# Optimization experiments

Hardware: AMD Instinct MI355X
Metric: run time of the kernel (lower is better)

## Reference

```python
import jax, jax.numpy as jnp
import numpy as np

N_NODES = 100000
N_ANGLES = 1000000
SCALAR_DIM = 128
ANGLE_ATTR_DIM = 2
HIDDEN = 64


def setup_inputs() -> dict:
    key = jax.random.key(0)
    ks = jax.random.split(key, 10)
    x = jax.random.normal(ks[0], (N_NODES, SCALAR_DIM), dtype=jnp.float32)
    triple_index = jax.random.randint(ks[1], (3, N_ANGLES), 0, N_NODES, dtype=jnp.int64)
    triple_attr = jax.random.normal(ks[2], (N_ANGLES, ANGLE_ATTR_DIM), dtype=jnp.float32)
    d_in = SCALAR_DIM * 2 + ANGLE_ATTR_DIM  # 258
    W1 = jax.random.normal(ks[3], (d_in, HIDDEN), dtype=jnp.float32) / np.sqrt(d_in)
    b1 = jnp.zeros((HIDDEN,), dtype=jnp.float32)
    W2 = jax.random.normal(ks[4], (HIDDEN, HIDDEN), dtype=jnp.float32) / np.sqrt(HIDDEN)
    b2 = jnp.zeros((HIDDEN,), dtype=jnp.float32)
    W3 = jax.random.normal(ks[5], (HIDDEN, SCALAR_DIM), dtype=jnp.float32) / np.sqrt(HIDDEN)
    b3 = jnp.zeros((SCALAR_DIM,), dtype=jnp.float32)
    # o3.Linear 128x0e -> 128x0e: bias-free dense linear with 1/sqrt(fan_in) norm
    Wout = jax.random.normal(ks[6], (SCALAR_DIM, SCALAR_DIM), dtype=jnp.float32) / np.sqrt(SCALAR_DIM)
    return {"x": x, "triple_index": triple_index, "triple_attr": triple_attr,
            "W1": W1, "b1": b1, "W2": W2, "b2": b2, "W3": W3, "b3": b3, "Wout": Wout}


def reference(x, triple_index, triple_attr, W1, b1, W2, b2, W3, b3, Wout):
    num_nodes = x.shape[0]
    x_scalar = x[:, :SCALAR_DIM]
    i, j, k = triple_index[0], triple_index[1], triple_index[2]
    # gather endpoints, concat with angle attrs: [E, 2*scalar_dim + 2]
    angle_input = jnp.concatenate([x_scalar[i], x_scalar[k], triple_attr], axis=-1)
    h = jax.nn.silu(angle_input @ W1 + b1)
    h = jax.nn.silu(h @ W2 + b2)
    msgs = h @ W3 + b3  # [E, scalar_dim]
    # scatter-mean by j
    sums = jax.ops.segment_sum(msgs, j, num_segments=num_nodes)
    cnts = jax.ops.segment_sum(jnp.ones((msgs.shape[0],), msgs.dtype), j, num_segments=num_nodes)
    aggr = sums / jnp.maximum(cnts, 1.0)[:, None]
    return aggr @ Wout
```

## Files before the change

### kernel.cpp

```cpp
#include <hip/hip_runtime.h>

#define NN 100000
#define NE 1000000
#define NBLK_SCAN 391

typedef float f4 __attribute__((ext_vector_type(4)));
typedef float f2 __attribute__((ext_vector_type(2)));
typedef _Float16 h8 __attribute__((ext_vector_type(8)));

__device__ __forceinline__ float silu(float v) {
    return v / (1.0f + __expf(-v));
}

#define O_SUMS   0
#define O_CNT    6400000
#define O_OFF    6500000
#define O_BSUM   6600000
#define O_BPRE   6600512
#define O_PERM   6601024
#define O_XA     7601024
#define O_XB     10801024
#define O_W3W    14001024
#define O_W2T    14009344

#define NODEPRE_B 3125
#define HIST_B    3907
#define W3W_B     33
#define PREP_B    (NODEPRE_B + HIST_B + W3W_B + 1)

__global__ __launch_bounds__(256) void k_prep(
    const float* __restrict__ x, const int* __restrict__ tj,
    const float* __restrict__ W1, const float* __restrict__ W2,
    const float* __restrict__ W3, const float* __restrict__ b3,
    const float* __restrict__ Wout,
    _Float16* __restrict__ XA, _Float16* __restrict__ XB,
    int* __restrict__ C, float* __restrict__ W3W, _Float16* __restrict__ W2t) {
    __shared__ float X[32][128];
    const int b = blockIdx.x;
    const int t = threadIdx.x;
    if (b < NODEPRE_B) {
        const int n0 = b * 32;
        const f4* xs = (const f4*)(x + (size_t)n0 * 128);
        f4* Xs = (f4*)&X[0][0];
#pragma unroll
        for (int q = 0; q < 4; ++q) Xs[t + 256 * q] = xs[t + 256 * q];
        __syncthreads();
        const int w = t >> 6, lane = t & 63;
        float aA[8], aB[8];
#pragma unroll
        for (int m = 0; m < 8; ++m) { aA[m] = 0.f; aB[m] = 0.f; }
        for (int d = 0; d < 128; ++d) {
            float wA = W1[d * 64 + lane];
            float wB = W1[(128 + d) * 64 + lane];
#pragma unroll
            for (int m = 0; m < 8; ++m) {
                float xv = X[w * 8 + m][d];
                aA[m] += xv * wA;
                aB[m] += xv * wB;
            }
        }
#pragma unroll
        for (int m = 0; m < 8; ++m) {
            XA[(size_t)(n0 + w * 8 + m) * 64 + lane] = (_Float16)aA[m];
            XB[(size_t)(n0 + w * 8 + m) * 64 + lane] = (_Float16)aB[m];
        }
    } else if (b < NODEPRE_B + HIST_B) {
        int e = (b - NODEPRE_B) * 256 + t;
        if (e < NE) atomicAdd(&C[tj[e]], 1);
    } else if (b < NODEPRE_B + HIST_B + W3W_B) {
        const int row = (b - NODEPRE_B - HIST_B) * 2 + (t >> 7);
        const int c = t & 127;
        if (row < 65) {
            const float* arow = (row < 64) ? (W3 + row * 128) : b3;
            float acc = 0.f;
            for (int d = 0; d < 128; ++d) acc += arow[d] * Wout[d * 128 + c];
            W3W[row * 128 + c] = acc;
        }
    } else {
#pragma unroll
        for (int u = 0; u < 16; ++u) {
            const int idx = t * 16 + u;
            const int n = idx >> 6, k = idx & 63;
            W2t[idx] = (_Float16)W2[k * 64 + n];
        }
    }
}

__global__ __launch_bounds__(256) void k_scan_local(const int* __restrict__ C,
                                                    int* __restrict__ offv,
                                                    int* __restrict__ Bsum) {
    __shared__ int s[256];
    const int t = threadIdx.x;
    const int gid = blockIdx.x * 256 + t;
    const int v = (gid < NN) ? C[gid] : 0;
    s[t] = v;
    __syncthreads();
    for (int off = 1; off < 256; off <<= 1) {
        int add = (t >= off) ? s[t - off] : 0;
        __syncthreads();
        s[t] += add;
        __syncthreads();
    }
    if (gid < NN) offv[gid] = s[t] - v;
    if (t == 255) Bsum[blockIdx.x] = s[255];
}

__global__ __launch_bounds__(512) void k_scan_block(const int* __restrict__ Bsum,
                                                    int* __restrict__ Bpre) {
    __shared__ int s[512];
    const int t = threadIdx.x;
    const int v = (t < NBLK_SCAN) ? Bsum[t] : 0;
    s[t] = v;
    __syncthreads();
    for (int off = 1; off < 512; off <<= 1) {
        int add = (t >= off) ? s[t - off] : 0;
        __syncthreads();
        s[t] += add;
        __syncthreads();
    }
    if (t < NBLK_SCAN) Bpre[t] = s[t] - v;
}

__global__ __launch_bounds__(256) void k_scatter(const int* __restrict__ tj,
                                                 const int* __restrict__ Bpre,
                                                 int* __restrict__ offv,
                                                 int* __restrict__ perm) {
    int e = blockIdx.x * 256 + threadIdx.x;
    if (e < NE) {
        int j = tj[e];
        int p = Bpre[j >> 8] + atomicAdd(&offv[j], 1);
        perm[p] = e;
    }
}

__global__ __launch_bounds__(256, 8) void k_edge(
    const int* __restrict__ ti, const int* __restrict__ tj, const int* __restrict__ tk,
    const int* __restrict__ perm, const float* __restrict__ attr,
    const _Float16* __restrict__ XA, const _Float16* __restrict__ XB,
    const float* __restrict__ W1, const float* __restrict__ b1,
    const _Float16* __restrict__ W2t, const float* __restrict__ b2,
    float* __restrict__ sums) {
    __shared__ __align__(16) char SBraw[64 * 68 * 4];
    __shared__ int JL[64];
    __shared__ int RS[66];
    __shared__ int nruns_s;

    _Float16* H1h = (_Float16*)SBraw;
    float* M = (float*)SBraw;

    const int t = threadIdx.x;
    const int w = t >> 6;
    const int lane = t & 63;
    const int EB = blockIdx.x * 64;

    {
        const int el = t >> 2;
        const int q = t & 3;
        const int e = perm[EB + el];
        const int i = ti[e];
        const int k = tk[e];
        if (q == 0) JL[el] = tj[e];
        f2 at = ((const f2*)attr)[e];
        const _Float16* xa = XA + (size_t)i * 64 + q * 16;
        const _Float16* xb = XB + (size_t)k * 64 + q * 16;
        h8 va0 = ((const h8*)xa)[0], va1 = ((const h8*)xa)[1];
        h8 vb0 = ((const h8*)xb)[0], vb1 = ((const h8*)xb)[1];
        float fa[16], fb[16];
#pragma unroll
        for (int n = 0; n < 8; ++n) {
            fa[n] = (float)va0[n]; fa[8 + n] = (float)va1[n];
            fb[n] = (float)vb0[n]; fb[8 + n] = (float)vb1[n];
        }
        const float* c0 = W1 + 256 * 64 + q * 16;
        const float* c1 = W1 + 257 * 64 + q * 16;
        const float* bq = b1 + q * 16;
        _Float16 hrow[16];
#pragma unroll
        for (int m4 = 0; m4 < 4; ++m4) {
            f4 vc0 = ((const f4*)c0)[m4];
            f4 vc1 = ((const f4*)c1)[m4];
            f4 vbq = ((const f4*)bq)[m4];
#pragma unroll
            for (int n = 0; n < 4; ++n) {
                const int idx = m4 * 4 + n;
                float pre = fa[idx] + fb[idx] + at[0] * vc0[n] + at[1] * vc1[n] + vbq[n];
                hrow[idx] = (_Float16)silu(pre);
            }
        }
        h8 s0, s1;
#pragma unroll
        for (int n = 0; n < 8; ++n) { s0[n] = hrow[n]; s1[n] = hrow[8 + n]; }
        _Float16* row = H1h + el * 72 + q * 16;
        ((h8*)row)[0] = s0;
        ((h8*)row)[1] = s1;
    }
    __syncthreads();

    const int r15 = lane & 15;
    const int blk = lane >> 4;
    float h2v[16];
    {
        const _Float16* H1w = H1h + (w * 16) * 72;
        h8 a0 = *(const h8*)(H1w + r15 * 72 + blk * 8);
        h8 a1 = *(const h8*)(H1w + r15 * 72 + 32 + blk * 8);
#pragma unroll
        for (int ncol = 0; ncol < 4; ++ncol) {
            const _Float16* Wn = W2t + (ncol * 16 + r15) * 64 + blk * 8;
            h8 b0 = *(const h8*)(Wn);
            h8 b1v = *(const h8*)(Wn + 32);
            const float bc = b2[ncol * 16 + r15];
            f4 acc = {bc, bc, bc, bc};
            acc = __builtin_amdgcn_mfma_f32_16x16x32_f16(a0, b0, acc, 0, 0, 0);
            acc = __builtin_amdgcn_mfma_f32_16x16x32_f16(a1, b1v, acc, 0, 0, 0);
#pragma unroll
            for (int reg = 0; reg < 4; ++reg) h2v[ncol * 4 + reg] = silu(acc[reg]);
        }
    }
    __syncthreads();

#pragma unroll
    for (int ncol = 0; ncol < 4; ++ncol)
#pragma unroll
        for (int reg = 0; reg < 4; ++reg)
            M[(w * 16 + blk * 4 + reg) * 68 + ncol * 16 + r15] = h2v[ncol * 4 + reg];
    if (t < 64) {
        bool head = (t == 0) || (JL[t] != JL[t - 1]);
        unsigned long long mask = __ballot(head);
        if (head) {
            int rank = __popcll(mask & ((1ull << t) - 1ull));
            RS[rank] = t;
        }
        if (t == 0) {
            int nr = __popcll(mask);
            nruns_s = nr;
            RS[nr] = 64;
        }
    }
    __syncthreads();

    {
        const int col = t & 63;
        const int q4 = t >> 6;
        const int nr = nruns_s;
        for (int rid = q4; rid < nr; rid += 4) {
            const int s0 = RS[rid];
            const int s1 = RS[rid + 1];
            float a = 0.f;
            for (int rr = s0; rr < s1; ++rr) a += M[rr * 68 + col];
            atomicAdd(&sums[(size_t)JL[s0] * 64 + col], a);
        }
    }
}

__global__ __launch_bounds__(256) void k_out(const float* __restrict__ sums,
                                             const int* __restrict__ C,
                                             const float* __restrict__ W3W,
                                             float* __restrict__ out) {
    __shared__ float S[32][64];
    __shared__ float bs[32];
    const int t = threadIdx.x;
    const int n0 = blockIdx.x * 32;
    const f4* ss = (const f4*)(sums + (size_t)n0 * 64);
    f4* Ss = (f4*)&S[0][0];
#pragma unroll
    for (int q = 0; q < 2; ++q) {
        const int fidx = t + 256 * q;
        const int row = fidx >> 4;
        const int cn = C[n0 + row];
        const float sc = (cn > 0) ? 1.0f / (float)cn : 0.0f;
        f4 v = ss[fidx];
#pragma unroll
        for (int n = 0; n < 4; ++n) v[n] *= sc;
        Ss[fidx] = v;
    }
    if (t < 32) bs[t] = (C[n0 + t] > 0) ? 1.0f : 0.0f;
    __syncthreads();
    const int w = t >> 6, lane = t & 63;
    const float* bout = W3W + 64 * 128;
    float a0[8], a1[8];
#pragma unroll
    for (int m = 0; m < 8; ++m) { a0[m] = 0.f; a1[m] = 0.f; }
    for (int d = 0; d < 64; ++d) {
        float w0 = W3W[d * 128 + lane];
        float w1 = W3W[d * 128 + 64 + lane];
#pragma unroll
        for (int m = 0; m < 8; ++m) {
            float sv = S[w * 8 + m][d];
            a0[m] += sv * w0;
            a1[m] += sv * w1;
        }
    }
    const float bo0 = bout[lane], bo1 = bout[64 + lane];
#pragma unroll
    for (int m = 0; m < 8; ++m) {
        const int node = n0 + w * 8 + m;
        const float b = bs[w * 8 + m];
        out[(size_t)node * 128 + lane] = a0[m] + b * bo0;
        out[(size_t)node * 128 + 64 + lane] = a1[m] + b * bo1;
    }
}

extern "C" void kernel_launch(void* const* d_in, const int* in_sizes, int n_in,
                              void* d_out, int out_size, void* d_ws, size_t ws_size,
                              hipStream_t stream) {
    const float* x    = (const float*)d_in[0];
    const int*   idx  = (const int*)d_in[1];
    const float* attr = (const float*)d_in[2];
    const float* W1   = (const float*)d_in[3];
    const float* b1   = (const float*)d_in[4];
    const float* W2   = (const float*)d_in[5];
    const float* b2   = (const float*)d_in[6];
    const float* W3   = (const float*)d_in[7];
    const float* b3   = (const float*)d_in[8];
    const float* Wout = (const float*)d_in[9];
    float* out = (float*)d_out;

    const int* ti = idx;
    const int* tj = idx + NE;
    const int* tk = idx + 2 * NE;

    float* ws   = (float*)d_ws;
    float* sums = ws + O_SUMS;
    int*   C    = (int*)(ws + O_CNT);
    int*   offv = (int*)(ws + O_OFF);
    int*   Bsum = (int*)(ws + O_BSUM);
    int*   Bpre = (int*)(ws + O_BPRE);
    int*   perm = (int*)(ws + O_PERM);
    _Float16* XA  = (_Float16*)(ws + O_XA);
    _Float16* XB  = (_Float16*)(ws + O_XB);
    float* W3W  = ws + O_W3W;
    _Float16* W2t = (_Float16*)(ws + O_W2T);

    hipMemsetAsync(sums, 0, (size_t)(6400000 + 100000) * sizeof(float), stream);

    hipLaunchKernelGGL(k_prep,       dim3(PREP_B), dim3(256), 0, stream,
                       x, tj, W1, W2, W3, b3, Wout, XA, XB, C, W3W, W2t);
    hipLaunchKernelGGL(k_scan_local, dim3(NBLK_SCAN), dim3(256), 0, stream, C, offv, Bsum);
    hipLaunchKernelGGL(k_scan_block, dim3(1), dim3(512), 0, stream, Bsum, Bpre);
    hipLaunchKernelGGL(k_scatter,    dim3(3907), dim3(256), 0, stream, tj, Bpre, offv, perm);
    hipLaunchKernelGGL(k_edge,       dim3(15625), dim3(256), 0, stream,
                       ti, tj, tk, perm, attr, XA, XB, W1, b1, W2t, b2, sums);
    hipLaunchKernelGGL(k_out,        dim3(3125), dim3(256), 0, stream, sums, C, W3W, out);
}
```

Before: 440.6 us.

## Use split-fp16 MFMA for node projection and fuse prep, scan and zeroing stages

Replaces the scalar FP32 node pre-projection (x @ W1 halves) with MFMA 16x16x32 fp16 instructions, using a hi/lo split of both x and W1 to keep near-fp32 accuracy. The histogram and weight prep stay in a first kernel. A new mid kernel merges the node projection with the local scan and with zeroing of the sums buffer, so the large memset is gone. The block-level scan is folded into k_scatter as a per-block wavefront scan, and nontemporal loads are added for the edge index streams. Together these cut launch count and FP32 ALU work, at the cost of three MFMAs per tile and some redundant scan work in every scatter block.

```diff
diff --git a/kernel.cpp b/kernel.cpp
--- a/kernel.cpp
+++ b/kernel.cpp
@@ -16,59 +16,34 @@
 #define O_CNT    6400000
 #define O_OFF    6500000
 #define O_BSUM   6600000
-#define O_BPRE   6600512
-#define O_PERM   6601024
-#define O_XA     7601024
-#define O_XB     10801024
-#define O_W3W    14001024
-#define O_W2T    14009344
-
-#define NODEPRE_B 3125
-#define HIST_B    3907
-#define W3W_B     33
-#define PREP_B    (NODEPRE_B + HIST_B + W3W_B + 1)
-
-__global__ __launch_bounds__(256) void k_prep(
-    const float* __restrict__ x, const int* __restrict__ tj,
+#define O_PERM   6600512
+#define O_XA     7600512
+#define O_XB     10800512
+#define O_W3W    14000512
+#define O_W2T    14008832
+#define O_W1TH   14010880
+#define O_W1TR   14019072
+
+#define HIST_B  3907
+#define W3W_B   33
+#define PREP0_B (HIST_B + W3W_B + 1 + 8)
+#define NPRE_B  1563
+#define MID_B   (NPRE_B + NBLK_SCAN)
+
+__global__ __launch_bounds__(256) void k_prep0(
+    const int* __restrict__ tj,
     const float* __restrict__ W1, const float* __restrict__ W2,
     const float* __restrict__ W3, const float* __restrict__ b3,
     const float* __restrict__ Wout,
-    _Float16* __restrict__ XA, _Float16* __restrict__ XB,
-    int* __restrict__ C, float* __restrict__ W3W, _Float16* __restrict__ W2t) {
-    __shared__ float X[32][128];
+    int* __restrict__ C, float* __restrict__ W3W, _Float16* __restrict__ W2t,
+    _Float16* __restrict__ W1th, _Float16* __restrict__ W1tr) {
     const int b = blockIdx.x;
     const int t = threadIdx.x;
-    if (b < NODEPRE_B) {
-        const int n0 = b * 32;
-        const f4* xs = (const f4*)(x + (size_t)n0 * 128);
-        f4* Xs = (f4*)&X[0][0];
-#pragma unroll
-        for (int q = 0; q < 4; ++q) Xs[t + 256 * q] = xs[t + 256 * q];
-        __syncthreads();
-        const int w = t >> 6, lane = t & 63;
-        float aA[8], aB[8];
-#pragma unroll
-        for (int m = 0; m < 8; ++m) { aA[m] = 0.f; aB[m] = 0.f; }
-        for (int d = 0; d < 128; ++d) {
-            float wA = W1[d * 64 + lane];
-            float wB = W1[(128 + d) * 64 + lane];
-#pragma unroll
-            for (int m = 0; m < 8; ++m) {
-                float xv = X[w * 8 + m][d];
-                aA[m] += xv * wA;
-                aB[m] += xv * wB;
-            }
-        }
-#pragma unroll
-        for (int m = 0; m < 8; ++m) {
-            XA[(size_t)(n0 + w * 8 + m) * 64 + lane] = (_Float16)aA[m];
-            XB[(size_t)(n0 + w * 8 + m) * 64 + lane] = (_Float16)aB[m];
-        }
-    } else if (b < NODEPRE_B + HIST_B) {
-        int e = (b - NODEPRE_B) * 256 + t;
-        if (e < NE) atomicAdd(&C[tj[e]], 1);
-    } else if (b < NODEPRE_B + HIST_B + W3W_B) {
-        const int row = (b - NODEPRE_B - HIST_B) * 2 + (t >> 7);
+    if (b < HIST_B) {
+        int e = b * 256 + t;
+        if (e < NE) atomicAdd(&C[__builtin_nontemporal_load(tj + e)], 1);
+    } else if (b < HIST_B + W3W_B) {
+        const int row = (b - HIST_B) * 2 + (t >> 7);
         const int c = t & 127;
         if (row < 65) {
             const float* arow = (row < 64) ? (W3 + row * 128) : b3;
@@ -76,59 +51,152 @@
             for (int d = 0; d < 128; ++d) acc += arow[d] * Wout[d * 128 + c];
             W3W[row * 128 + c] = acc;
         }
-    } else {
+    } else if (b < HIST_B + W3W_B + 1) {
 #pragma unroll
         for (int u = 0; u < 16; ++u) {
             const int idx = t * 16 + u;
             const int n = idx >> 6, k = idx & 63;
             W2t[idx] = (_Float16)W2[k * 64 + n];
         }
-    }
-}
-
-__global__ __launch_bounds__(256) void k_scan_local(const int* __restrict__ C,
-                                                    int* __restrict__ offv,
-                                                    int* __restrict__ Bsum) {
+    } else {
+        const int b0 = b - (HIST_B + W3W_B + 1);
+#pragma unroll
+        for (int u = 0; u < 8; ++u) {
+            const int idx = b0 * 2048 + t * 8 + u;
+            const int np = idx >> 7, k = idx & 127;
+            const float wfull = W1[(k + ((np >= 64) ? 128 : 0)) * 64 + (np & 63)];
+            const _Float16 wh = (_Float16)wfull;
+            W1th[idx] = wh;
+            W1tr[idx] = (_Float16)(wfull - (float)wh);
+        }
+    }
+}
+
+__global__ __launch_bounds__(256) void k_mid(
+    const float* __restrict__ x,
+    const _Float16* __restrict__ W1th, const _Float16* __restrict__ W1tr,
+    _Float16* __restrict__ XA, _Float16* __restrict__ XB,
+    const int* __restrict__ C, float* __restrict__ sums,
+    int* __restrict__ offv, int* __restrict__ Bsum) {
+    __shared__ _Float16 XOUT[2][64][72];
     __shared__ int s[256];
+    const int b = blockIdx.x;
     const int t = threadIdx.x;
-    const int gid = blockIdx.x * 256 + t;
-    const int v = (gid < NN) ? C[gid] : 0;
-    s[t] = v;
-    __syncthreads();
-    for (int off = 1; off < 256; off <<= 1) {
-        int add = (t >= off) ? s[t - off] : 0;
+    if (b < NPRE_B) {
+        const int n0 = b * 64;
+        const int w = t >> 6;
+        const int lane = t & 63;
+        const int r15 = lane & 15, blk = lane >> 4;
+        const int nodeRow = n0 + w * 16 + r15;
+        const bool rowOK = nodeRow < NN;
+        f4 accA[4], accB[4];
+#pragma unroll
+        for (int n = 0; n < 4; ++n) {
+            accA[n] = (f4){0.f, 0.f, 0.f, 0.f};
+            accB[n] = (f4){0.f, 0.f, 0.f, 0.f};
+        }
+#pragma unroll
+        for (int kk = 0; kk < 4; ++kk) {
+            f4 x0 = (f4){0.f, 0.f, 0.f, 0.f}, x1 = x0;
+            if (rowOK) {
+                const f4* xp = (const f4*)(x + (size_t)nodeRow * 128 + kk * 32 + blk * 8);
+                x0 = xp[0];
+                x1 = xp[1];
+            }
+            h8 xh, xr;
+#pragma unroll
+            for (int n = 0; n < 4; ++n) {
+                xh[n] = (_Float16)x0[n];
+                xr[n] = (_Float16)(x0[n] - (float)xh[n]);
+                xh[4 + n] = (_Float16)x1[n];
+                xr[4 + n] = (_Float16)(x1[n] - (float)xh[4 + n]);
+            }
+#pragma unroll
+            for (int ncol = 0; ncol < 4; ++ncol) {
+                const int nA = ncol * 16 + r15;
+                const int koff = kk * 32 + blk * 8;
+                h8 whA = *(const h8*)(W1th + nA * 128 + koff);
+                h8 wrA = *(const h8*)(W1tr + nA * 128 + koff);
+                accA[ncol] = __builtin_amdgcn_mfma_f32_16x16x32_f16(xh, whA, accA[ncol], 0, 0, 0);
+                accA[ncol] = __builtin_amdgcn_mfma_f32_16x16x32_f16(xr, whA, accA[ncol], 0, 0, 0);
+                accA[ncol] = __builtin_amdgcn_mfma_f32_16x16x32_f16(xh, wrA, accA[ncol], 0, 0, 0);
+                h8 whB = *(const h8*)(W1th + (64 + nA) * 128 + koff);
+                h8 wrB = *(const h8*)(W1tr + (64 + nA) * 128 + koff);
+                accB[ncol] = __builtin_amdgcn_mfma_f32_16x16x32_f16(xh, whB, accB[ncol], 0, 0, 0);
+                accB[ncol] = __builtin_amdgcn_mfma_f32_16x16x32_f16(xr, whB, accB[ncol], 0, 0, 0);
+                accB[ncol] = __builtin_amdgcn_mfma_f32_16x16x32_f16(xh, wrB, accB[ncol], 0, 0, 0);
+            }
+        }
+#pragma unroll
+        for (int ncol = 0; ncol < 4; ++ncol)
+#pragma unroll
+            for (int reg = 0; reg < 4; ++reg) {
+                const int row = w * 16 + blk * 4 + reg;
+                XOUT[0][row][ncol * 16 + r15] = (_Float16)accA[ncol][reg];
+                XOUT[1][row][ncol * 16 + r15] = (_Float16)accB[ncol][reg];
+            }
         __syncthreads();
-        s[t] += add;
+#pragma unroll
+        for (int u = 0; u < 4; ++u) {
+            const int idx = t + 256 * u;
+            const int mat = idx >> 9;
+            const int row = (idx >> 3) & 63;
+            const int c8 = idx & 7;
+            const int grow = n0 + row;
+            if (grow < NN) {
+                _Float16* dst = (mat ? XB : XA) + (size_t)grow * 64 + c8 * 8;
+                *(h8*)dst = *(const h8*)&XOUT[mat][row][c8 * 8];
+            }
+        }
+    } else {
+        const int sb = b - NPRE_B;
+        {
+            f4* sz = (f4*)sums + (size_t)sb * 4096;
+            const int cnt4 = min(4096, 1600000 - sb * 4096);
+            for (int u = t; u < cnt4; u += 256) sz[u] = (f4){0.f, 0.f, 0.f, 0.f};
+        }
+        const int gid = sb * 256 + t;
+        const int v = (gid < NN) ? C[gid] : 0;
+        s[t] = v;
         __syncthreads();
-    }
-    if (gid < NN) offv[gid] = s[t] - v;
-    if (t == 255) Bsum[blockIdx.x] = s[255];
-}
-
-__global__ __launch_bounds__(512) void k_scan_block(const int* __restrict__ Bsum,
-                                                    int* __restrict__ Bpre) {
-    __shared__ int s[512];
-    const int t = threadIdx.x;
-    const int v = (t < NBLK_SCAN) ? Bsum[t] : 0;
-    s[t] = v;
-    __syncthreads();
-    for (int off = 1; off < 512; off <<= 1) {
-        int add = (t >= off) ? s[t - off] : 0;
-        __syncthreads();
-        s[t] += add;
-        __syncthreads();
-    }
-    if (t < NBLK_SCAN) Bpre[t] = s[t] - v;
+        for (int off = 1; off < 256; off <<= 1) {
+            int add = (t >= off) ? s[t - off] : 0;
+            __syncthreads();
+            s[t] += add;
+            __syncthreads();
+        }
+        if (gid < NN) offv[gid] = s[t] - v;
+        if (t == 255) Bsum[sb] = s[255];
+    }
 }
 
 __global__ __launch_bounds__(256) void k_scatter(const int* __restrict__ tj,
-                                                 const int* __restrict__ Bpre,
+                                                 const int* __restrict__ Bsum,
                                                  int* __restrict__ offv,
                                                  int* __restrict__ perm) {
-    int e = blockIdx.x * 256 + threadIdx.x;
+    __shared__ int BpreS[NBLK_SCAN];
+    const int t = threadIdx.x;
+    const int w = t >> 6, lane = t & 63;
+    if (w == 0) {
+        int carry = 0;
+        for (int base = 0; base < NBLK_SCAN; base += 64) {
+            const int idx = base + lane;
+            const int orig = (idx < NBLK_SCAN) ? Bsum[idx] : 0;
+            int v = orig;
+#pragma unroll
+            for (int off = 1; off < 64; off <<= 1) {
+                int u = __shfl_up(v, off, 64);
+                if (lane >= off) v += u;
+            }
+            if (idx < NBLK_SCAN) BpreS[idx] = carry + v - orig;
+            carry += __shfl(v, 63, 64);
+        }
+    }
+    __syncthreads();
+    const int e = blockIdx.x * 256 + t;
     if (e < NE) {
-        int j = tj[e];
-        int p = Bpre[j >> 8] + atomicAdd(&offv[j], 1);
+        const int j = __builtin_nontemporal_load(tj + e);
+        const int p = BpreS[j >> 8] + atomicAdd(&offv[j], 1);
         perm[p] = e;
     }
 }
@@ -156,11 +224,11 @@
     {
         const int el = t >> 2;
         const int q = t & 3;
-        const int e = perm[EB + el];
-        const int i = ti[e];
-        const int k = tk[e];
-        if (q == 0) JL[el] = tj[e];
-        f2 at = ((const f2*)attr)[e];
+        const int e = __builtin_nontemporal_load(perm + EB + el);
+        const int i = __builtin_nontemporal_load(ti + e);
+        const int k = __builtin_nontemporal_load(tk + e);
+        if (q == 0) JL[el] = __builtin_nontemporal_load(tj + e);
+        f2 at = __builtin_nontemporal_load((const f2*)attr + e);
         const _Float16* xa = XA + (size_t)i * 64 + q * 16;
         const _Float16* xb = XB + (size_t)k * 64 + q * 16;
         h8 va0 = ((const h8*)xa)[0], va1 = ((const h8*)xa)[1];
@@ -324,21 +392,22 @@
     int*   C    = (int*)(ws + O_CNT);
     int*   offv = (int*)(ws + O_OFF);
     int*   Bsum = (int*)(ws + O_BSUM);
-    int*   Bpre = (int*)(ws + O_BPRE);
     int*   perm = (int*)(ws + O_PERM);
     _Float16* XA  = (_Float16*)(ws + O_XA);
     _Float16* XB  = (_Float16*)(ws + O_XB);
     float* W3W  = ws + O_W3W;
-    _Float16* W2t = (_Float16*)(ws + O_W2T);
-
-    hipMemsetAsync(sums, 0, (size_t)(6400000 + 100000) * sizeof(float), stream);
-
-    hipLaunchKernelGGL(k_prep,       dim3(PREP_B), dim3(256), 0, stream,
-                       x, tj, W1, W2, W3, b3, Wout, XA, XB, C, W3W, W2t);
-    hipLaunchKernelGGL(k_scan_local, dim3(NBLK_SCAN), dim3(256), 0, stream, C, offv, Bsum);
-    hipLaunchKernelGGL(k_scan_block, dim3(1), dim3(512), 0, stream, Bsum, Bpre);
-    hipLaunchKernelGGL(k_scatter,    dim3(3907), dim3(256), 0, stream, tj, Bpre, offv, perm);
-    hipLaunchKernelGGL(k_edge,       dim3(15625), dim3(256), 0, stream,
+    _Float16* W2t  = (_Float16*)(ws + O_W2T);
+    _Float16* W1th = (_Float16*)(ws + O_W1TH);
+    _Float16* W1tr = (_Float16*)(ws + O_W1TR);
+
+    hipMemsetAsync(C, 0, (size_t)NN * sizeof(int), stream);
+
+    hipLaunchKernelGGL(k_prep0,   dim3(PREP0_B), dim3(256), 0, stream,
+                       tj, W1, W2, W3, b3, Wout, C, W3W, W2t, W1th, W1tr);
+    hipLaunchKernelGGL(k_mid,     dim3(MID_B), dim3(256), 0, stream,
+                       x, W1th, W1tr, XA, XB, C, sums, offv, Bsum);
+    hipLaunchKernelGGL(k_scatter, dim3(3907), dim3(256), 0, stream, tj, Bsum, offv, perm);
+    hipLaunchKernelGGL(k_edge,    dim3(15625), dim3(256), 0, stream,
                        ti, tj, tk, perm, attr, XA, XB, W1, b1, W2t, b2, sums);
-    hipLaunchKernelGGL(k_out,        dim3(3125), dim3(256), 0, stream, sums, C, W3W, out);
-}
+    hipLaunchKernelGGL(k_out,     dim3(3125), dim3(256), 0, stream, sums, C, W3W, out);
+}
```

After: 475.0 us. +7.8%, slower.
